# Optimization experiments

Hardware: AMD Instinct MI355X
Metric: run time of the kernel (lower is better)

## Reference

```python
import jax, jax.numpy as jnp
import numpy as np
import math

B, S, HID = 2, 2048, 1024
D = 64            # size_per_head
H = HID // D      # num heads = 16
ROT = 32          # rotary_hsize = size_per_head // 2


def _apply_rotary(qk, sinusoids):
    # qk: [B, S, H, D]; sinusoids: [B, 2, S, ROT]
    sin = sinusoids[:, 0, :, None, :]   # [B, S, 1, ROT]
    cos = sinusoids[:, 1, :, None, :]
    qk_rope = qk[..., :ROT]
    # torch.stack([-a[..., ::2], a[..., 1::2]], -1).reshape(a.shape)
    rot2 = jnp.stack([-qk_rope[..., ::2], qk_rope[..., 1::2]], axis=-1).reshape(qk_rope.shape)
    qk_rope = qk_rope * cos + rot2 * sin
    return jnp.concatenate([qk_rope, qk[..., ROT:]], axis=-1)


def setup_inputs() -> dict:
    key = jax.random.key(0)
    ks = jax.random.split(key, 8)
    sc = 1.0 / math.sqrt(HID)
    return {
        "x": jax.random.normal(ks[0], (B, S, HID), jnp.float32),
        "sinusoids": jax.random.normal(ks[1], (B, 2, S, ROT), jnp.float32),
        "attention_bias": jax.random.uniform(ks[2], (B, 1, S, S), jnp.float32),
        "Wq": jax.random.normal(ks[3], (HID, HID), jnp.float32) * sc,
        "bq": jnp.zeros((HID,), jnp.float32),
        "Wk": jax.random.normal(ks[4], (HID, HID), jnp.float32) * sc,
        "bk": jnp.zeros((HID,), jnp.float32),
        "Wv": jax.random.normal(ks[5], (HID, HID), jnp.float32) * sc,
        "bv": jnp.zeros((HID,), jnp.float32),
        "Wo": jax.random.normal(ks[6], (HID, HID), jnp.float32) * sc,
    }


def reference(x, sinusoids, attention_bias, Wq, bq, Wk, bk, Wv, bv, Wo):
    q = (x @ Wq + bq).reshape(B, S, H, D)
    k = (x @ Wk + bk).reshape(B, S, H, D)
    v = (x @ Wv + bv).reshape(B, S, H, D)
    # original concatenates q,k along the heads dim before rotary; since rotary
    # broadcasts over heads, applying it to each separately is identical math
    q = _apply_rotary(q, sinusoids)
    k = _apply_rotary(k, sinusoids)
    q = q / math.sqrt(D)
    scores = jnp.einsum('bqhd,bkhd->bhqk', q, k)          # [B,H,S,S]
    probs = jax.nn.softmax(scores, axis=-1)
    probs = probs * attention_bias                         # multiplicative bias AFTER softmax
    out = jnp.einsum('bhqk,bkhd->bqhd', probs, v)          # [B,S,H,D]
    out = out.reshape(B, S, HID)
    return out @ Wo
```

## Files before the change

### kernel.cpp

```cpp
#include <hip/hip_runtime.h>
#include <math.h>

#define B_   2
#define S_   2048
#define HID_ 1024
#define D_   64
#define H_   16
#define ROT_ 32
#define M_   (B_*S_)

typedef __attribute__((ext_vector_type(4))) short  short4v;
typedef __attribute__((ext_vector_type(8))) short  short8;
typedef __attribute__((ext_vector_type(4))) float  floatx4;
typedef __attribute__((ext_vector_type(16))) float floatx16;
typedef __attribute__((ext_vector_type(2))) unsigned int uint2v;

__device__ __forceinline__ unsigned short f2bf(float f) {
  unsigned int x = __builtin_bit_cast(unsigned int, f);
  x += 0x7fffu + ((x >> 16) & 1u);
  return (unsigned short)(x >> 16);
}
__device__ __forceinline__ unsigned int cvt_pk_bf16(float lo, float hi) {
  unsigned int r;
  asm("v_cvt_pk_bf16_f32 %0, %1, %2" : "=v"(r) : "v"(lo), "v"(hi));
  return r;
}
__device__ __forceinline__ void gload_lds16(const unsigned short* g, unsigned short* l) {
  __builtin_amdgcn_global_load_lds(
      (const __attribute__((address_space(1))) unsigned int*)g,
      (__attribute__((address_space(3))) unsigned int*)l, 16, 0, 0);
}

__global__ void cast_bf16(const float* __restrict__ in, unsigned short* __restrict__ out) {
  int i = (blockIdx.x * 256 + threadIdx.x) * 4;
  floatx4 v = *(const floatx4*)(in + i);
  unsigned short o[4];
  o[0] = f2bf(v[0]); o[1] = f2bf(v[1]); o[2] = f2bf(v[2]); o[3] = f2bf(v[3]);
  *(unsigned long long*)(out + i) = *(unsigned long long*)o;
}

__global__ void transW(const float* __restrict__ W0, const float* __restrict__ W1,
                       const float* __restrict__ W2, const float* __restrict__ W3,
                       unsigned short* __restrict__ T0, unsigned short* __restrict__ T1,
                       unsigned short* __restrict__ T2, unsigned short* __restrict__ T3) {
  const float* W; unsigned short* T;
  int z = blockIdx.z;
  if (z == 0)      { W = W0; T = T0; }
  else if (z == 1) { W = W1; T = T1; }
  else if (z == 2) { W = W2; T = T2; }
  else             { W = W3; T = T3; }
  __shared__ float tile[32][33];
  int bx = blockIdx.x * 32, by = blockIdx.y * 32;
  int tx = threadIdx.x, ty = threadIdx.y;
  #pragma unroll
  for (int j = 0; j < 4; j++)
    tile[ty + j*8][tx] = W[(size_t)(by + ty + j*8) * HID_ + bx + tx];
  __syncthreads();
  #pragma unroll
  for (int j = 0; j < 4; j++)
    T[(size_t)(bx + ty + j*8) * HID_ + by + tx] = f2bf(tile[tx][ty + j*8]);
}

template <int MODE>
__global__ __launch_bounds__(256) void gemm_bt(
    const unsigned short* __restrict__ A,
    const unsigned short* __restrict__ Bt0, const unsigned short* __restrict__ Bt1,
    const unsigned short* __restrict__ Bt2,
    const float* __restrict__ bias0, const float* __restrict__ bias1,
    const float* __restrict__ bias2,
    void* __restrict__ out0, void* __restrict__ out1, void* __restrict__ out2,
    const float* __restrict__ sins, float sc0)
{
  const unsigned short* Bt; const float* bias; void* Out; float sc;
  if (blockIdx.z == 0)      { Bt = Bt0; bias = bias0; Out = out0; sc = sc0; }
  else if (blockIdx.z == 1) { Bt = Bt1; bias = bias1; Out = out1; sc = 1.f; }
  else                      { Bt = Bt2; bias = bias2; Out = out2; sc = 1.f; }
  const int K = HID_, N = HID_;
  int m0 = blockIdx.y * 128, n0 = blockIdx.x * 128;
  __shared__ alignas(16) unsigned short sA[3][128 * 32];
  __shared__ alignas(16) unsigned short sB[3][128 * 32];
  int t = threadIdx.x;
  int lane = t & 63, wave = t >> 6;
  int quad = lane >> 4, l16 = lane & 15;
  int wr = wave >> 1, wc = wave & 1;

  int srow = (lane >> 2), scol = (lane & 3) * 8;
  const unsigned short* gA0 = A  + (size_t)(m0 + wave*32 +  0 + srow) * K + scol;
  const unsigned short* gA1 = A  + (size_t)(m0 + wave*32 + 16 + srow) * K + scol;
  const unsigned short* gB0 = Bt + (size_t)(n0 + wave*32 +  0 + srow) * K + scol;
  const unsigned short* gB1 = Bt + (size_t)(n0 + wave*32 + 16 + srow) * K + scol;

#define GSTAGE(bi, k0) do { \
    gload_lds16(gA0 + (k0), sA[bi] + (wave*32 +  0) * 32); \
    gload_lds16(gA1 + (k0), sA[bi] + (wave*32 + 16) * 32); \
    gload_lds16(gB0 + (k0), sB[bi] + (wave*32 +  0) * 32); \
    gload_lds16(gB1 + (k0), sB[bi] + (wave*32 + 16) * 32); \
  } while (0)

  floatx4 acc[4][4];
  #pragma unroll
  for (int i = 0; i < 4; i++)
    #pragma unroll
    for (int j = 0; j < 4; j++)
      acc[i][j] = (floatx4){0.f, 0.f, 0.f, 0.f};

  const int NK = K / 32;
  GSTAGE(0, 0);
  GSTAGE(1, 32);
  for (int ks = 0; ks < NK; ks++) {
    int cur = ks % 3;
    if (ks + 1 < NK) asm volatile("s_waitcnt vmcnt(4)" ::: "memory");
    else             asm volatile("s_waitcnt vmcnt(0)" ::: "memory");
    __builtin_amdgcn_s_barrier();
    __builtin_amdgcn_sched_barrier(0);
    if (ks + 2 < NK) GSTAGE((ks + 2) % 3, (ks + 2) * 32);

    short8 af[4], bf[4];
    #pragma unroll
    for (int i = 0; i < 4; i++) {
      af[i] = *(const short8*)(sA[cur] + (wr * 64 + i * 16 + l16) * 32 + quad * 8);
      bf[i] = *(const short8*)(sB[cur] + (wc * 64 + i * 16 + l16) * 32 + quad * 8);
    }
    #pragma unroll
    for (int i = 0; i < 4; i++)
      #pragma unroll
      for (int j = 0; j < 4; j++)
        acc[i][j] = __builtin_amdgcn_mfma_f32_16x16x32_bf16(af[i], bf[j], acc[i][j], 0, 0, 0);
  }
#undef GSTAGE

  #pragma unroll
  for (int i = 0; i < 4; i++) {
    int mbase = m0 + wr * 64 + i * 16 + quad * 4;
    #pragma unroll
    for (int j = 0; j < 4; j++) {
      int n = n0 + wc * 64 + j * 16 + l16;
      float bv = bias ? bias[n] : 0.f;
      if (MODE == 1) {
        #pragma unroll
        for (int r = 0; r < 4; r++)
          ((float*)Out)[(size_t)(mbase + r) * N + n] = acc[i][j][r] + bv;
      } else if (blockIdx.z == 2) {
        int bb = mbase >> 11, ss = mbase & 2047;
        int hh = n >> 6, dd = n & 63;
        unsigned short pk[4];
        #pragma unroll
        for (int r = 0; r < 4; r++) pk[r] = f2bf(acc[i][j][r] + bv);
        *(unsigned long long*)((unsigned short*)Out +
            (((size_t)(bb * H_ + hh) * D_ + dd) * S_ + ss)) = *(unsigned long long*)pk;
      } else if (j < 2) {
        int jh = j * 16 + l16;
        #pragma unroll
        for (int r = 0; r < 4; r++) {
          int row = mbase + r, bb = row >> 11, ss = row & 2047;
          float sn = sins[((size_t)(bb * 2 + 0) * S_ + ss) * ROT_ + jh];
          float cs = sins[((size_t)(bb * 2 + 1) * S_ + ss) * ROT_ + jh];
          float f = (jh & 1) ? (cs + sn) : (cs - sn);
          ((unsigned short*)Out)[(size_t)row * N + n] = f2bf((acc[i][j][r] + bv) * f * sc);
        }
      } else {
        #pragma unroll
        for (int r = 0; r < 4; r++)
          ((unsigned short*)Out)[(size_t)(mbase + r) * N + n] = f2bf((acc[i][j][r] + bv) * sc);
      }
    }
  }
}

__global__ __launch_bounds__(256) void gemm_bt64(
    const unsigned short* __restrict__ A, const unsigned short* __restrict__ Bt,
    float* __restrict__ Out)
{
  const int K = HID_, N = HID_;
  int m0 = blockIdx.y * 128, n0 = blockIdx.x * 64;
  __shared__ alignas(16) unsigned short sA[3][128 * 32];
  __shared__ alignas(16) unsigned short sB[3][64 * 32];
  int t = threadIdx.x;
  int lane = t & 63, wave = t >> 6;
  int quad = lane >> 4, l16 = lane & 15;
  int wr = wave >> 1, wc = wave & 1;

  int srow = lane >> 2, scol = (lane & 3) * 8;
  const unsigned short* gA0 = A  + (size_t)(m0 + wave*32 +  0 + srow) * K + scol;
  const unsigned short* gA1 = A  + (size_t)(m0 + wave*32 + 16 + srow) * K + scol;
  const unsigned short* gB0 = Bt + (size_t)(n0 + wave*16 + srow) * K + scol;

#define GSTAGE(bi, k0) do { \
    gload_lds16(gA0 + (k0), sA[bi] + (wave*32 +  0) * 32); \
    gload_lds16(gA1 + (k0), sA[bi] + (wave*32 + 16) * 32); \
    gload_lds16(gB0 + (k0), sB[bi] + (wave*16) * 32); \
  } while (0)

  floatx4 acc[4][2];
  #pragma unroll
  for (int i = 0; i < 4; i++)
    #pragma unroll
    for (int j = 0; j < 2; j++)
      acc[i][j] = (floatx4){0.f, 0.f, 0.f, 0.f};

  const int NK = K / 32;
  GSTAGE(0, 0);
  GSTAGE(1, 32);
  for (int ks = 0; ks < NK; ks++) {
    int cur = ks % 3;
    if (ks + 1 < NK) asm volatile("s_waitcnt vmcnt(3)" ::: "memory");
    else             asm volatile("s_waitcnt vmcnt(0)" ::: "memory");
    __builtin_amdgcn_s_barrier();
    __builtin_amdgcn_sched_barrier(0);
    if (ks + 2 < NK) GSTAGE((ks + 2) % 3, (ks + 2) * 32);

    short8 af[4], bf[2];
    #pragma unroll
    for (int i = 0; i < 4; i++)
      af[i] = *(const short8*)(sA[cur] + (wr * 64 + i * 16 + l16) * 32 + quad * 8);
    #pragma unroll
    for (int j = 0; j < 2; j++)
      bf[j] = *(const short8*)(sB[cur] + (wc * 32 + j * 16 + l16) * 32 + quad * 8);
    #pragma unroll
    for (int i = 0; i < 4; i++)
      #pragma unroll
      for (int j = 0; j < 2; j++)
        acc[i][j] = __builtin_amdgcn_mfma_f32_16x16x32_bf16(af[i], bf[j], acc[i][j], 0, 0, 0);
  }
#undef GSTAGE

  #pragma unroll
  for (int i = 0; i < 4; i++) {
    int mbase = m0 + wr * 64 + i * 16 + quad * 4;
    #pragma unroll
    for (int j = 0; j < 2; j++) {
      int n = n0 + wc * 32 + j * 16 + l16;
      #pragma unroll
      for (int r = 0; r < 4; r++)
        Out[(size_t)(mbase + r) * N + n] = acc[i][j][r];
    }
  }
}

__global__ __launch_bounds__(512, 1) void attn(
    const unsigned short* __restrict__ Q, const unsigned short* __restrict__ Kb,
    const unsigned short* __restrict__ Vt, const float* __restrict__ bias,
    unsigned short* __restrict__ Out)
{
  int b = blockIdx.z, h = blockIdx.y;
  int t = threadIdx.x;
  int lane = t & 63, wave = t >> 6;
  int g = wave >> 2, wg = wave & 3;
  int l32 = lane & 31, hl = lane >> 5;
  int s7 = l32 & 7;
  int q0 = blockIdx.x * 128 + wg * 32;
  const int RS = H_ * D_;
  const int NT = S_ / 128;

  __shared__ alignas(16) unsigned short smem[65536];
  unsigned short* bg = smem + g * 32768;

  const unsigned short* Qbase = Q + ((size_t)(b * S_) * H_ + h) * D_;
  const unsigned short* Kbase = Kb + ((size_t)(b * S_) * H_ + h) * D_;
  const unsigned short* Vbase = Vt + ((size_t)(b * H_) + h) * D_ * S_;

  short8 qf[4];
  {
    const unsigned short* qp = Qbase + (size_t)(q0 + l32) * RS + 8 * hl;
    qf[0] = *(const short8*)(qp);
    qf[1] = *(const short8*)(qp + 16);
    qf[2] = *(const short8*)(qp + 32);
    qf[3] = *(const short8*)(qp + 48);
  }

  int tg = t & 255;
  int row0 = tg >> 3;
  int csw  = (tg & 7) ^ (row0 & 7);
  const unsigned short* gK0 = Kbase + (size_t)(g*1024 + row0)      * RS + csw * 8;
  const unsigned short* gK1 = Kbase + (size_t)(g*1024 + row0 + 32) * RS + csw * 8;
  const unsigned short* gV0 = Vbase + (size_t)(row0)      * S_ + g*1024 + csw * 8;
  const unsigned short* gV1 = Vbase + (size_t)(row0 + 32) * S_ + g*1024 + csw * 8;

  const float* bp = bias + (size_t)b * S_ * S_ + (size_t)(q0 + l32) * S_ + g * 1024 + 4 * hl;

#define STAGE(bi, tk) do { \
    unsigned short* kb_ = bg + (bi) * 4096; \
    unsigned short* vb_ = bg + 16384 + (bi) * 4096; \
    size_t ko_ = (size_t)(tk) * 64 * RS; int vo_ = (tk) * 64; \
    gload_lds16(gK0 + ko_, kb_ + tg * 8); \
    gload_lds16(gK1 + ko_, kb_ + (256 + tg) * 8); \
    gload_lds16(gV0 + vo_, vb_ + tg * 8); \
    gload_lds16(gV1 + vo_, vb_ + (256 + tg) * 8); \
  } while (0)

  float l_run = 0.f;
  floatx16 o0, o1;
  #pragma unroll
  for (int r = 0; r < 16; r++) { o0[r] = 0.f; o1[r] = 0.f; }

  STAGE(0, 0);
  floatx4 b0[4], b1[4];
  #pragma unroll
  for (int rg = 0; rg < 4; rg++) {
    b0[rg] = *(const floatx4*)(bp + 8 * rg);
    b1[rg] = *(const floatx4*)(bp + 32 + 8 * rg);
  }
  STAGE(1, 1);
  STAGE(2, 2);

  for (int it = 0; it < NT; ++it) {
    int cur = it & 3;
    asm volatile("s_waitcnt vmcnt(16)" ::: "memory");
    __builtin_amdgcn_s_barrier();
    __builtin_amdgcn_sched_barrier(0);
    if (it < NT - 3) STAGE((it + 3) & 3, it + 3);

    const unsigned short* kbuf = bg + cur * 4096;
    const unsigned short* vbuf = bg + 16384 + cur * 4096;
    int itn = ((it + 1) & (NT - 1)) * 64;

    floatx16 st;
    #pragma unroll
    for (int r = 0; r < 16; r++) st[r] = 0.f;
    __builtin_amdgcn_s_setprio(1);
    #pragma unroll
    for (int ks = 0; ks < 4; ks++) {
      short8 kf = *(const short8*)(kbuf + l32 * 64 + (((2 * ks + hl) ^ s7) * 8));
      st = __builtin_amdgcn_mfma_f32_32x32x16_bf16(kf, qf[ks], st, 0, 0, 0);
    }
    __builtin_amdgcn_s_setprio(0);

    short4v pf0[4];
    #pragma unroll
    for (int rg = 0; rg < 4; rg++) {
      float p0 = __builtin_amdgcn_exp2f(st[rg * 4 + 0]);
      float p1 = __builtin_amdgcn_exp2f(st[rg * 4 + 1]);
      float p2 = __builtin_amdgcn_exp2f(st[rg * 4 + 2]);
      float p3 = __builtin_amdgcn_exp2f(st[rg * 4 + 3]);
      l_run += (p0 + p1) + (p2 + p3);
      uint2v u;
      u[0] = cvt_pk_bf16(p0 * b0[rg][0], p1 * b0[rg][1]);
      u[1] = cvt_pk_bf16(p2 * b0[rg][2], p3 * b0[rg][3]);
      pf0[rg] = __builtin_bit_cast(short4v, u);
    }
    #pragma unroll
    for (int rg = 0; rg < 4; rg++)
      b0[rg] = *(const floatx4*)(bp + itn + 8 * rg);

    floatx16 st1;
    #pragma unroll
    for (int r = 0; r < 16; r++) st1[r] = 0.f;
    __builtin_amdgcn_s_setprio(1);
    #pragma unroll
    for (int ks = 0; ks < 4; ks++) {
      short8 kf = *(const short8*)(kbuf + (32 + l32) * 64 + (((2 * ks + hl) ^ s7) * 8));
      st1 = __builtin_amdgcn_mfma_f32_32x32x16_bf16(kf, qf[ks], st1, 0, 0, 0);
    }
    #pragma unroll
    for (int gg = 0; gg < 4; gg++) {
      int ch = (gg ^ s7) * 8 + hl * 4;
      short4v vf0 = *(const short4v*)(vbuf + l32 * 64 + ch);
      short4v vf1 = *(const short4v*)(vbuf + (32 + l32) * 64 + ch);
      o0 = __builtin_amdgcn_mfma_f32_32x32x8bf16_1k(pf0[gg], vf0, o0, 0, 0, 0);
      o1 = __builtin_amdgcn_mfma_f32_32x32x8bf16_1k(pf0[gg], vf1, o1, 0, 0, 0);
    }
    __builtin_amdgcn_s_setprio(0);

    short4v pf1[4];
    #pragma unroll
    for (int rg = 0; rg < 4; rg++) {
      float p0 = __builtin_amdgcn_exp2f(st1[rg * 4 + 0]);
      float p1 = __builtin_amdgcn_exp2f(st1[rg * 4 + 1]);
      float p2 = __builtin_amdgcn_exp2f(st1[rg * 4 + 2]);
      float p3 = __builtin_amdgcn_exp2f(st1[rg * 4 + 3]);
      l_run += (p0 + p1) + (p2 + p3);
      uint2v u;
      u[0] = cvt_pk_bf16(p0 * b1[rg][0], p1 * b1[rg][1]);
      u[1] = cvt_pk_bf16(p2 * b1[rg][2], p3 * b1[rg][3]);
      pf1[rg] = __builtin_bit_cast(short4v, u);
    }
    #pragma unroll
    for (int rg = 0; rg < 4; rg++)
      b1[rg] = *(const floatx4*)(bp + itn + 32 + 8 * rg);

    __builtin_amdgcn_s_setprio(1);
    #pragma unroll
    for (int gg = 0; gg < 4; gg++) {
      int ch = ((4 + gg) ^ s7) * 8 + hl * 4;
      short4v vf0 = *(const short4v*)(vbuf + l32 * 64 + ch);
      short4v vf1 = *(const short4v*)(vbuf + (32 + l32) * 64 + ch);
      o0 = __builtin_amdgcn_mfma_f32_32x32x8bf16_1k(pf1[gg], vf0, o0, 0, 0, 0);
      o1 = __builtin_amdgcn_mfma_f32_32x32x8bf16_1k(pf1[gg], vf1, o1, 0, 0, 0);
    }
    __builtin_amdgcn_s_setprio(0);
  }
#undef STAGE

  float l2 = l_run + __shfl_xor(l_run, 32);

  float* sO = (float*)smem;
  float* sL = (float*)(smem + 16384);

  __syncthreads();
  if (g == 1) {
    #pragma unroll
    for (int r = 0; r < 16; r++) {
      int ql = (r & 3) + 8 * (r >> 2) + 4 * hl;
      sO[(wg * 32 + ql) * 64 + l32]      = o0[r];
      sO[(wg * 32 + ql) * 64 + 32 + l32] = o1[r];
    }
    if (hl == 0) sL[wg * 32 + l32] = l2;
  }
  __syncthreads();
  if (g == 0) {
    float linv = __builtin_amdgcn_rcpf(l2 + sL[wg * 32 + l32]);
    #pragma unroll
    for (int r = 0; r < 16; r++) {
      int ql = (r & 3) + 8 * (r >> 2) + 4 * hl;
      float sc = __shfl(linv, ql);
      size_t base = ((size_t)(b * S_ + q0 + ql) * H_ + h) * D_;
      float a0 = o0[r] + sO[(wg * 32 + ql) * 64 + l32];
      float a1 = o1[r] + sO[(wg * 32 + ql) * 64 + 32 + l32];
      Out[base + l32]      = f2bf(a0 * sc);
      Out[base + 32 + l32] = f2bf(a1 * sc);
    }
  }
}

extern "C" void kernel_launch(void* const* d_in, const int* in_sizes, int n_in,
                              void* d_out, int out_size, void* d_ws, size_t ws_size,
                              hipStream_t stream) {
  (void)in_sizes; (void)n_in; (void)out_size; (void)ws_size;
  const float* x    = (const float*)d_in[0];
  const float* sins = (const float*)d_in[1];
  const float* ab   = (const float*)d_in[2];
  const float* Wq   = (const float*)d_in[3];
  const float* bq   = (const float*)d_in[4];
  const float* Wk   = (const float*)d_in[5];
  const float* bk   = (const float*)d_in[6];
  const float* Wv   = (const float*)d_in[7];
  const float* bv   = (const float*)d_in[8];
  const float* Wo   = (const float*)d_in[9];
  float* out = (float*)d_out;
  char* ws = (char*)d_ws;

  unsigned short* xb  = (unsigned short*)(ws);
  unsigned short* Wqt = (unsigned short*)(ws + ((size_t) 8 << 20));
  unsigned short* Wkt = (unsigned short*)(ws + ((size_t)10 << 20));
  unsigned short* Wvt = (unsigned short*)(ws + ((size_t)12 << 20));
  unsigned short* Wot = (unsigned short*)(ws + ((size_t)14 << 20));
  unsigned short* Qb  = (unsigned short*)(ws + ((size_t)16 << 20));
  unsigned short* Kb  = (unsigned short*)(ws + ((size_t)24 << 20));
  unsigned short* Vtb = (unsigned short*)(ws + ((size_t)32 << 20));
  unsigned short* Ab  = (unsigned short*)(ws + ((size_t)40 << 20));

  const float c1 = 0.125f * 1.44269504088896f;

  cast_bf16<<<dim3((M_ * HID_) / (256 * 4)), dim3(256), 0, stream>>>(x, xb);
  transW<<<dim3(32, 32, 4), dim3(32, 8), 0, stream>>>(Wq, Wk, Wv, Wo, Wqt, Wkt, Wvt, Wot);
  gemm_bt<0><<<dim3(8, 32, 3), dim3(256), 0, stream>>>(xb, Wqt, Wkt, Wvt, bq, bk, bv,
                                                       Qb, Kb, Vtb, sins, c1);
  attn<<<dim3(S_ / 128, H_, B_), dim3(512), 0, stream>>>(Qb, Kb, Vtb, ab, Ab);
  gemm_bt64<<<dim3(HID_ / 64, M_ / 128), dim3(256), 0, stream>>>(Ab, Wot, out);
}
```

Baseline: 258.6 us.

## Process two heads per attention block to reuse bias loads across heads

Each attention workgroup now handles a pair of heads, so the fp32 attention-bias tile loaded for a query/key block is used for both heads instead of being reread per head. The grid halves to 8 head-pairs, and the K/V staging moves from a 4-deep ring of single-head tiles to a double buffer holding both heads. This is meant to halve global bias traffic, which is the largest input stream. In exchange the prefetch pipeline is shallower, register pressure roughly doubles for the accumulators and Q fragments, and there are half as many blocks to fill the GPU.

```diff
diff --git a/kernel.cpp b/kernel.cpp
--- a/kernel.cpp
+++ b/kernel.cpp
@@ -242,7 +242,8 @@
     const unsigned short* __restrict__ Vt, const float* __restrict__ bias,
     unsigned short* __restrict__ Out)
 {
-  int b = blockIdx.z, h = blockIdx.y;
+  int b = blockIdx.z, hp = blockIdx.y;
+  int h0 = hp * 2;
   int t = threadIdx.x;
   int lane = t & 63, wave = t >> 6;
   int g = wave >> 2, wg = wave & 3;
@@ -251,21 +252,23 @@
   int q0 = blockIdx.x * 128 + wg * 32;
   const int RS = H_ * D_;
   const int NT = S_ / 128;
+  const int VH = D_ * S_;
 
   __shared__ alignas(16) unsigned short smem[65536];
   unsigned short* bg = smem + g * 32768;
 
-  const unsigned short* Qbase = Q + ((size_t)(b * S_) * H_ + h) * D_;
-  const unsigned short* Kbase = Kb + ((size_t)(b * S_) * H_ + h) * D_;
-  const unsigned short* Vbase = Vt + ((size_t)(b * H_) + h) * D_ * S_;
-
-  short8 qf[4];
-  {
-    const unsigned short* qp = Qbase + (size_t)(q0 + l32) * RS + 8 * hl;
-    qf[0] = *(const short8*)(qp);
-    qf[1] = *(const short8*)(qp + 16);
-    qf[2] = *(const short8*)(qp + 32);
-    qf[3] = *(const short8*)(qp + 48);
+  const unsigned short* Qbase = Q + ((size_t)(b * S_) * H_ + h0) * D_;
+  const unsigned short* Kbase = Kb + ((size_t)(b * S_) * H_ + h0) * D_;
+  const unsigned short* Vbase = Vt + ((size_t)(b * H_) + h0) * D_ * S_;
+
+  short8 qf[2][4];
+  #pragma unroll
+  for (int H = 0; H < 2; H++) {
+    const unsigned short* qp = Qbase + (size_t)(q0 + l32) * RS + H * D_ + 8 * hl;
+    qf[H][0] = *(const short8*)(qp);
+    qf[H][1] = *(const short8*)(qp + 16);
+    qf[H][2] = *(const short8*)(qp + 32);
+    qf[H][3] = *(const short8*)(qp + 48);
   }
 
   int tg = t & 255;
@@ -279,19 +282,22 @@
   const float* bp = bias + (size_t)b * S_ * S_ + (size_t)(q0 + l32) * S_ + g * 1024 + 4 * hl;
 
 #define STAGE(bi, tk) do { \
-    unsigned short* kb_ = bg + (bi) * 4096; \
-    unsigned short* vb_ = bg + 16384 + (bi) * 4096; \
+    unsigned short* base_ = bg + (bi) * 16384; \
     size_t ko_ = (size_t)(tk) * 64 * RS; int vo_ = (tk) * 64; \
-    gload_lds16(gK0 + ko_, kb_ + tg * 8); \
-    gload_lds16(gK1 + ko_, kb_ + (256 + tg) * 8); \
-    gload_lds16(gV0 + vo_, vb_ + tg * 8); \
-    gload_lds16(gV1 + vo_, vb_ + (256 + tg) * 8); \
+    gload_lds16(gK0 + ko_,        base_ + tg * 8); \
+    gload_lds16(gK1 + ko_,        base_ + (256 + tg) * 8); \
+    gload_lds16(gK0 + ko_ + 64,   base_ + 4096 + tg * 8); \
+    gload_lds16(gK1 + ko_ + 64,   base_ + 4096 + (256 + tg) * 8); \
+    gload_lds16(gV0 + vo_,        base_ + 8192 + tg * 8); \
+    gload_lds16(gV1 + vo_,        base_ + 8192 + (256 + tg) * 8); \
+    gload_lds16(gV0 + vo_ + VH,   base_ + 12288 + tg * 8); \
+    gload_lds16(gV1 + vo_ + VH,   base_ + 12288 + (256 + tg) * 8); \
   } while (0)
 
-  float l_run = 0.f;
-  floatx16 o0, o1;
-  #pragma unroll
-  for (int r = 0; r < 16; r++) { o0[r] = 0.f; o1[r] = 0.f; }
+  float lr0 = 0.f, lr1 = 0.f;
+  floatx16 o00, o01, o10, o11;
+  #pragma unroll
+  for (int r = 0; r < 16; r++) { o00[r] = 0.f; o01[r] = 0.f; o10[r] = 0.f; o11[r] = 0.f; }
 
   STAGE(0, 0);
   floatx4 b0[4], b1[4];
@@ -300,124 +306,139 @@
     b0[rg] = *(const floatx4*)(bp + 8 * rg);
     b1[rg] = *(const floatx4*)(bp + 32 + 8 * rg);
   }
-  STAGE(1, 1);
-  STAGE(2, 2);
 
   for (int it = 0; it < NT; ++it) {
-    int cur = it & 3;
-    asm volatile("s_waitcnt vmcnt(16)" ::: "memory");
+    int cur = it & 1;
+    asm volatile("s_waitcnt vmcnt(8)" ::: "memory");
     __builtin_amdgcn_s_barrier();
     __builtin_amdgcn_sched_barrier(0);
-    if (it < NT - 3) STAGE((it + 3) & 3, it + 3);
-
-    const unsigned short* kbuf = bg + cur * 4096;
-    const unsigned short* vbuf = bg + 16384 + cur * 4096;
+    if (it < NT - 1) STAGE(cur ^ 1, it + 1);
+    __builtin_amdgcn_sched_barrier(0);
+
     int itn = ((it + 1) & (NT - 1)) * 64;
 
-    floatx16 st;
-    #pragma unroll
-    for (int r = 0; r < 16; r++) st[r] = 0.f;
-    __builtin_amdgcn_s_setprio(1);
-    #pragma unroll
-    for (int ks = 0; ks < 4; ks++) {
-      short8 kf = *(const short8*)(kbuf + l32 * 64 + (((2 * ks + hl) ^ s7) * 8));
-      st = __builtin_amdgcn_mfma_f32_32x32x16_bf16(kf, qf[ks], st, 0, 0, 0);
-    }
-    __builtin_amdgcn_s_setprio(0);
-
-    short4v pf0[4];
-    #pragma unroll
-    for (int rg = 0; rg < 4; rg++) {
-      float p0 = __builtin_amdgcn_exp2f(st[rg * 4 + 0]);
-      float p1 = __builtin_amdgcn_exp2f(st[rg * 4 + 1]);
-      float p2 = __builtin_amdgcn_exp2f(st[rg * 4 + 2]);
-      float p3 = __builtin_amdgcn_exp2f(st[rg * 4 + 3]);
-      l_run += (p0 + p1) + (p2 + p3);
-      uint2v u;
-      u[0] = cvt_pk_bf16(p0 * b0[rg][0], p1 * b0[rg][1]);
-      u[1] = cvt_pk_bf16(p2 * b0[rg][2], p3 * b0[rg][3]);
-      pf0[rg] = __builtin_bit_cast(short4v, u);
-    }
-    #pragma unroll
-    for (int rg = 0; rg < 4; rg++)
-      b0[rg] = *(const floatx4*)(bp + itn + 8 * rg);
-
-    floatx16 st1;
-    #pragma unroll
-    for (int r = 0; r < 16; r++) st1[r] = 0.f;
-    __builtin_amdgcn_s_setprio(1);
-    #pragma unroll
-    for (int ks = 0; ks < 4; ks++) {
-      short8 kf = *(const short8*)(kbuf + (32 + l32) * 64 + (((2 * ks + hl) ^ s7) * 8));
-      st1 = __builtin_amdgcn_mfma_f32_32x32x16_bf16(kf, qf[ks], st1, 0, 0, 0);
-    }
-    #pragma unroll
-    for (int gg = 0; gg < 4; gg++) {
-      int ch = (gg ^ s7) * 8 + hl * 4;
-      short4v vf0 = *(const short4v*)(vbuf + l32 * 64 + ch);
-      short4v vf1 = *(const short4v*)(vbuf + (32 + l32) * 64 + ch);
-      o0 = __builtin_amdgcn_mfma_f32_32x32x8bf16_1k(pf0[gg], vf0, o0, 0, 0, 0);
-      o1 = __builtin_amdgcn_mfma_f32_32x32x8bf16_1k(pf0[gg], vf1, o1, 0, 0, 0);
-    }
-    __builtin_amdgcn_s_setprio(0);
-
-    short4v pf1[4];
-    #pragma unroll
-    for (int rg = 0; rg < 4; rg++) {
-      float p0 = __builtin_amdgcn_exp2f(st1[rg * 4 + 0]);
-      float p1 = __builtin_amdgcn_exp2f(st1[rg * 4 + 1]);
-      float p2 = __builtin_amdgcn_exp2f(st1[rg * 4 + 2]);
-      float p3 = __builtin_amdgcn_exp2f(st1[rg * 4 + 3]);
-      l_run += (p0 + p1) + (p2 + p3);
-      uint2v u;
-      u[0] = cvt_pk_bf16(p0 * b1[rg][0], p1 * b1[rg][1]);
-      u[1] = cvt_pk_bf16(p2 * b1[rg][2], p3 * b1[rg][3]);
-      pf1[rg] = __builtin_bit_cast(short4v, u);
-    }
-    #pragma unroll
-    for (int rg = 0; rg < 4; rg++)
-      b1[rg] = *(const floatx4*)(bp + itn + 32 + 8 * rg);
-
-    __builtin_amdgcn_s_setprio(1);
-    #pragma unroll
-    for (int gg = 0; gg < 4; gg++) {
-      int ch = ((4 + gg) ^ s7) * 8 + hl * 4;
-      short4v vf0 = *(const short4v*)(vbuf + l32 * 64 + ch);
-      short4v vf1 = *(const short4v*)(vbuf + (32 + l32) * 64 + ch);
-      o0 = __builtin_amdgcn_mfma_f32_32x32x8bf16_1k(pf1[gg], vf0, o0, 0, 0, 0);
-      o1 = __builtin_amdgcn_mfma_f32_32x32x8bf16_1k(pf1[gg], vf1, o1, 0, 0, 0);
-    }
-    __builtin_amdgcn_s_setprio(0);
+    #pragma unroll
+    for (int H = 0; H < 2; H++) {
+      const unsigned short* kbuf = bg + cur * 16384 + H * 4096;
+      const unsigned short* vbuf = bg + cur * 16384 + 8192 + H * 4096;
+      floatx16& oa = H ? o10 : o00;
+      floatx16& ob = H ? o11 : o01;
+      float& lr = H ? lr1 : lr0;
+
+      floatx16 st;
+      #pragma unroll
+      for (int r = 0; r < 16; r++) st[r] = 0.f;
+      __builtin_amdgcn_s_setprio(1);
+      #pragma unroll
+      for (int ks = 0; ks < 4; ks++) {
+        short8 kf = *(const short8*)(kbuf + l32 * 64 + (((2 * ks + hl) ^ s7) * 8));
+        st = __builtin_amdgcn_mfma_f32_32x32x16_bf16(kf, qf[H][ks], st, 0, 0, 0);
+      }
+      __builtin_amdgcn_s_setprio(0);
+
+      short4v pf0[4];
+      #pragma unroll
+      for (int rg = 0; rg < 4; rg++) {
+        float p0 = __builtin_amdgcn_exp2f(st[rg * 4 + 0]);
+        float p1 = __builtin_amdgcn_exp2f(st[rg * 4 + 1]);
+        float p2 = __builtin_amdgcn_exp2f(st[rg * 4 + 2]);
+        float p3 = __builtin_amdgcn_exp2f(st[rg * 4 + 3]);
+        lr += (p0 + p1) + (p2 + p3);
+        uint2v u;
+        u[0] = cvt_pk_bf16(p0 * b0[rg][0], p1 * b0[rg][1]);
+        u[1] = cvt_pk_bf16(p2 * b0[rg][2], p3 * b0[rg][3]);
+        pf0[rg] = __builtin_bit_cast(short4v, u);
+      }
+      if (H == 1) {
+        #pragma unroll
+        for (int rg = 0; rg < 4; rg++)
+          b0[rg] = *(const floatx4*)(bp + itn + 8 * rg);
+      }
+
+      floatx16 st1;
+      #pragma unroll
+      for (int r = 0; r < 16; r++) st1[r] = 0.f;
+      __builtin_amdgcn_s_setprio(1);
+      #pragma unroll
+      for (int ks = 0; ks < 4; ks++) {
+        short8 kf = *(const short8*)(kbuf + (32 + l32) * 64 + (((2 * ks + hl) ^ s7) * 8));
+        st1 = __builtin_amdgcn_mfma_f32_32x32x16_bf16(kf, qf[H][ks], st1, 0, 0, 0);
+      }
+      #pragma unroll
+      for (int gg = 0; gg < 4; gg++) {
+        int ch = (gg ^ s7) * 8 + hl * 4;
+        short4v vf0 = *(const short4v*)(vbuf + l32 * 64 + ch);
+        short4v vf1 = *(const short4v*)(vbuf + (32 + l32) * 64 + ch);
+        oa = __builtin_amdgcn_mfma_f32_32x32x8bf16_1k(pf0[gg], vf0, oa, 0, 0, 0);
+        ob = __builtin_amdgcn_mfma_f32_32x32x8bf16_1k(pf0[gg], vf1, ob, 0, 0, 0);
+      }
+      __builtin_amdgcn_s_setprio(0);
+
+      short4v pf1[4];
+      #pragma unroll
+      for (int rg = 0; rg < 4; rg++) {
+        float p0 = __builtin_amdgcn_exp2f(st1[rg * 4 + 0]);
+        float p1 = __builtin_amdgcn_exp2f(st1[rg * 4 + 1]);
+        float p2 = __builtin_amdgcn_exp2f(st1[rg * 4 + 2]);
+        float p3 = __builtin_amdgcn_exp2f(st1[rg * 4 + 3]);
+        lr += (p0 + p1) + (p2 + p3);
+        uint2v u;
+        u[0] = cvt_pk_bf16(p0 * b1[rg][0], p1 * b1[rg][1]);
+        u[1] = cvt_pk_bf16(p2 * b1[rg][2], p3 * b1[rg][3]);
+        pf1[rg] = __builtin_bit_cast(short4v, u);
+      }
+      if (H == 1) {
+        #pragma unroll
+        for (int rg = 0; rg < 4; rg++)
+          b1[rg] = *(const floatx4*)(bp + itn + 32 + 8 * rg);
+      }
+
+      __builtin_amdgcn_s_setprio(1);
+      #pragma unroll
+      for (int gg = 0; gg < 4; gg++) {
+        int ch = ((4 + gg) ^ s7) * 8 + hl * 4;
+        short4v vf0 = *(const short4v*)(vbuf + l32 * 64 + ch);
+        short4v vf1 = *(const short4v*)(vbuf + (32 + l32) * 64 + ch);
+        oa = __builtin_amdgcn_mfma_f32_32x32x8bf16_1k(pf1[gg], vf0, oa, 0, 0, 0);
+        ob = __builtin_amdgcn_mfma_f32_32x32x8bf16_1k(pf1[gg], vf1, ob, 0, 0, 0);
+      }
+      __builtin_amdgcn_s_setprio(0);
+    }
   }
 #undef STAGE
-
-  float l2 = l_run + __shfl_xor(l_run, 32);
 
   float* sO = (float*)smem;
   float* sL = (float*)(smem + 16384);
 
-  __syncthreads();
-  if (g == 1) {
-    #pragma unroll
-    for (int r = 0; r < 16; r++) {
-      int ql = (r & 3) + 8 * (r >> 2) + 4 * hl;
-      sO[(wg * 32 + ql) * 64 + l32]      = o0[r];
-      sO[(wg * 32 + ql) * 64 + 32 + l32] = o1[r];
-    }
-    if (hl == 0) sL[wg * 32 + l32] = l2;
-  }
-  __syncthreads();
-  if (g == 0) {
-    float linv = __builtin_amdgcn_rcpf(l2 + sL[wg * 32 + l32]);
-    #pragma unroll
-    for (int r = 0; r < 16; r++) {
-      int ql = (r & 3) + 8 * (r >> 2) + 4 * hl;
-      float sc = __shfl(linv, ql);
-      size_t base = ((size_t)(b * S_ + q0 + ql) * H_ + h) * D_;
-      float a0 = o0[r] + sO[(wg * 32 + ql) * 64 + l32];
-      float a1 = o1[r] + sO[(wg * 32 + ql) * 64 + 32 + l32];
-      Out[base + l32]      = f2bf(a0 * sc);
-      Out[base + 32 + l32] = f2bf(a1 * sc);
+  #pragma unroll
+  for (int H = 0; H < 2; H++) {
+    floatx16& oa = H ? o10 : o00;
+    floatx16& ob = H ? o11 : o01;
+    float l2 = (H ? lr1 : lr0) + __shfl_xor(H ? lr1 : lr0, 32);
+
+    __syncthreads();
+    if (g == 1) {
+      #pragma unroll
+      for (int r = 0; r < 16; r++) {
+        int ql = (r & 3) + 8 * (r >> 2) + 4 * hl;
+        sO[(wg * 32 + ql) * 64 + l32]      = oa[r];
+        sO[(wg * 32 + ql) * 64 + 32 + l32] = ob[r];
+      }
+      if (hl == 0) sL[wg * 32 + l32] = l2;
+    }
+    __syncthreads();
+    if (g == 0) {
+      float linv = __builtin_amdgcn_rcpf(l2 + sL[wg * 32 + l32]);
+      #pragma unroll
+      for (int r = 0; r < 16; r++) {
+        int ql = (r & 3) + 8 * (r >> 2) + 4 * hl;
+        float sc = __shfl(linv, ql);
+        size_t base = ((size_t)(b * S_ + q0 + ql) * H_ + h0 + H) * D_;
+        float a0 = oa[r] + sO[(wg * 32 + ql) * 64 + l32];
+        float a1 = ob[r] + sO[(wg * 32 + ql) * 64 + 32 + l32];
+        Out[base + l32]      = f2bf(a0 * sc);
+        Out[base + 32 + l32] = f2bf(a1 * sc);
+      }
     }
   }
 }
@@ -455,6 +476,6 @@
   transW<<<dim3(32, 32, 4), dim3(32, 8), 0, stream>>>(Wq, Wk, Wv, Wo, Wqt, Wkt, Wvt, Wot);
   gemm_bt<0><<<dim3(8, 32, 3), dim3(256), 0, stream>>>(xb, Wqt, Wkt, Wvt, bq, bk, bv,
                                                        Qb, Kb, Vtb, sins, c1);
-  attn<<<dim3(S_ / 128, H_, B_), dim3(512), 0, stream>>>(Qb, Kb, Vtb, ab, Ab);
+  attn<<<dim3(S_ / 128, H_ / 2, B_), dim3(512), 0, stream>>>(Qb, Kb, Vtb, ab, Ab);
   gemm_bt64<<<dim3(HID_ / 64, M_ / 128), dim3(256), 0, stream>>>(Ab, Wot, out);
 }
```

New measurement: 263.8 us. 1.02x slower.
